# Kernel tuning notes

Measured on AMD Instinct MI355X. Metric: run time of the kernel, lower is better.

## Reference

```python
import jax, jax.numpy as jnp
import numpy as np

B, N, D, H, FF = 4, 1024, 512, 8, 2048
DH = D // H
RPE_HID = 16
COORD_DIM = 2


def _ln(x, g, b, eps=1e-5):
    m = jnp.mean(x, axis=-1, keepdims=True)
    v = jnp.mean((x - m) ** 2, axis=-1, keepdims=True)
    return (x - m) * jax.lax.rsqrt(v + eps) * g + b


def setup_inputs() -> dict:
    key = jax.random.key(0)
    ks = jax.random.split(key, 20)
    s = 0.02
    inp = {
        "x": jax.random.normal(ks[0], (B, N, D), dtype=jnp.float32),
        "coords": jax.random.uniform(ks[1], (B, N, COORD_DIM), dtype=jnp.float32),
        # qkv + output projections
        "Wq": jax.random.normal(ks[2], (D, D), jnp.float32) * s,
        "bq": jnp.zeros((D,), jnp.float32),
        "Wk": jax.random.normal(ks[3], (D, D), jnp.float32) * s,
        "bk": jnp.zeros((D,), jnp.float32),
        "Wv": jax.random.normal(ks[4], (D, D), jnp.float32) * s,
        "bv": jnp.zeros((D,), jnp.float32),
        "Wo": jax.random.normal(ks[5], (D, D), jnp.float32) * s,
        "bo": jnp.zeros((D,), jnp.float32),
        # learned per-head logit scale (Swin-v2 style cosine attention)
        "logit_scale": jnp.full((H, 1, 1), np.log(10.0), jnp.float32),
        # absolute positional embedder PE: Linear(2 -> D)
        "W_pe": jax.random.normal(ks[6], (COORD_DIM, D), jnp.float32) * s,
        "b_pe": jnp.zeros((D,), jnp.float32),
        # relative positional embedder RPE: MLP(2 -> 16 -> H)
        "W_r1": jax.random.normal(ks[7], (COORD_DIM, RPE_HID), jnp.float32) * 0.5,
        "b_r1": jnp.zeros((RPE_HID,), jnp.float32),
        "W_r2": jax.random.normal(ks[8], (RPE_HID, H), jnp.float32) * 0.5,
        "b_r2": jnp.zeros((H,), jnp.float32),
        # layernorm params
        "g_peq": jnp.ones((D,), jnp.float32), "bt_peq": jnp.zeros((D,), jnp.float32),
        "g_pek": jnp.ones((D,), jnp.float32), "bt_pek": jnp.zeros((D,), jnp.float32),
        "g2": jnp.ones((D,), jnp.float32), "bt2": jnp.zeros((D,), jnp.float32),
        "g3": jnp.ones((D,), jnp.float32), "bt3": jnp.zeros((D,), jnp.float32),
        # MLP (bias=False)
        "W_ff1": jax.random.normal(ks[9], (D, FF), jnp.float32) * s,
        "W_ff2": jax.random.normal(ks[10], (FF, D), jnp.float32) * s,
    }
    return inp


def reference(x, coords, Wq, bq, Wk, bk, Wv, bv, Wo, bo, logit_scale,
              W_pe, b_pe, W_r1, b_r1, W_r2, b_r2,
              g_peq, bt_peq, g_pek, bt_pek, g2, bt2, g3, bt3,
              W_ff1, W_ff2):
    # --- PE add + LayerNorm on q and k (self-attention: coords_cross_ = coords)
    pe = coords @ W_pe + b_pe                      # [B,N,D]
    q = _ln(x + pe, g_peq, bt_peq)
    k = _ln(x + pe, g_pek, bt_pek)
    v = x                                          # v is NOT PE-normed in source

    # --- relative-position bias from cartesian coord differences
    rel = coords[:, :, None, :] - coords[:, None, :, :]   # [B,Nq,Nk,2]
    hid = jax.nn.relu(rel @ W_r1 + b_r1)                  # [B,Nq,Nk,16]
    bias = hid @ W_r2 + b_r2                              # [B,Nq,Nk,H]
    bias = jnp.transpose(bias, (0, 3, 1, 2))              # [B,H,Nq,Nk]

    # --- multi-head cosine attention with learned logit scale
    qp = (q @ Wq + bq).reshape(B, N, H, DH)
    kp = (k @ Wk + bk).reshape(B, N, H, DH)
    vp = (v @ Wv + bv).reshape(B, N, H, DH)
    qn = qp / jnp.maximum(jnp.linalg.norm(qp, axis=-1, keepdims=True), 1e-12)
    kn = kp / jnp.maximum(jnp.linalg.norm(kp, axis=-1, keepdims=True), 1e-12)
    scale = jnp.exp(jnp.minimum(logit_scale, jnp.log(100.0)))  # [H,1,1]
    attn = jnp.einsum('bqhd,bkhd->bhqk', qn, kn) * scale[None] + bias
    attn = jax.nn.softmax(attn, axis=-1)
    att_out = jnp.einsum('bhqk,bkhd->bqhd', attn, vp).reshape(B, N, D)
    att_out = att_out @ Wo + bo

    # --- residual + norm + MLP (LeakyReLU 0.2 after each linear) + residual + norm
    x1 = _ln(x + att_out, g2, bt2)
    mlp = jax.nn.leaky_relu(
        jax.nn.leaky_relu(x1 @ W_ff1, 0.2) @ W_ff2, 0.2)
    return _ln(x1 + mlp, g3, bt3)
```

## Files before the change

### kernel.cpp

```cpp
#include <hip/hip_runtime.h>

#define BB 4
#define NN 1024
#define DD 512
#define HH 8
#define DHH 64
#define FFF 2048

typedef __attribute__((ext_vector_type(8))) short bf16x8;
typedef __attribute__((ext_vector_type(4))) float f32x4;
typedef __attribute__((ext_vector_type(4))) unsigned short u16x4;

__device__ inline float wave_sum(float v) {
#pragma unroll
  for (int off = 32; off; off >>= 1) v += __shfl_xor(v, off);
  return v;
}

__device__ inline unsigned short cvt_bf16(float f) {
  union { float f; unsigned u; } x;
  x.f = f;
  unsigned r = x.u + 0x7FFFu + ((x.u >> 16) & 1u);
  return (unsigned short)(r >> 16);
}

__device__ __forceinline__ void gl_lds16(const void* g, void* l) {
  __builtin_amdgcn_global_load_lds(
      (__attribute__((address_space(1))) void*)(g),
      (__attribute__((address_space(3))) void*)(l), 16, 0, 0);
}

__global__ __launch_bounds__(256) void wconv_kernel(
    const float* __restrict__ W0, const float* __restrict__ W1,
    const float* __restrict__ W2, const float* __restrict__ W3,
    const float* __restrict__ W4, const float* __restrict__ W5,
    unsigned short* __restrict__ out) {
  int bidx = blockIdx.x;
  const float* W; unsigned short* Wt; int K, N, local;
  if (bidx < 256) {
    int sel = bidx >> 6; local = bidx & 63;
    W = sel == 0 ? W0 : sel == 1 ? W1 : sel == 2 ? W2 : W3;
    K = 512; N = 512; Wt = out + (size_t)sel * 262144;
  } else if (bidx < 512) {
    local = bidx - 256; W = W4; K = 512; N = 2048; Wt = out + 1048576;
  } else {
    local = bidx - 512; W = W5; K = 2048; N = 512; Wt = out + 2097152;
  }
  int ntn = N >> 6;
  int tn = (local & (ntn - 1)) << 6, tk = (local / ntn) << 6;
  __shared__ float tile[64][65];
  int tid = threadIdx.x;
#pragma unroll
  for (int i = 0; i < 16; ++i) {
    int e = tid + i * 256, kk = e >> 6, nn = e & 63;
    tile[kk][nn] = W[(size_t)(tk + kk) * N + tn + nn];
  }
  __syncthreads();
#pragma unroll
  for (int i = 0; i < 16; ++i) {
    int e = tid + i * 256, nn = e >> 6, kk = e & 63;
    Wt[(size_t)(tn + nn) * K + tk + kk] = cvt_bf16(tile[kk][nn]);
  }
}

__global__ __launch_bounds__(256) void bias_kernel(
    const float* __restrict__ coords,
    const float* __restrict__ W_r1, const float* __restrict__ b_r1,
    const float* __restrict__ W_r2, const float* __restrict__ b_r2,
    unsigned short* __restrict__ bias_out, float* __restrict__ rowmax_out) {
  int kt = blockIdx.x, qt = blockIdx.y, b = blockIdx.z;
  int tid = threadIdx.x;
  int qL = tid >> 2;
  int q = qt * 64 + qL;
  int k0 = kt * 32 + (tid & 3) * 8;
  float cq0 = coords[((size_t)b * NN + q) * 2 + 0];
  float cq1 = coords[((size_t)b * NN + q) * 2 + 1];
  float Aq[16];
#pragma unroll
  for (int l = 0; l < 16; ++l)
    Aq[l] = fmaf(cq0, W_r1[l], fmaf(cq1, W_r1[16 + l], b_r1[l]));
  float ck0[8], ck1[8];
#pragma unroll
  for (int kk = 0; kk < 8; ++kk) {
    ck0[kk] = coords[((size_t)b * NN + k0 + kk) * 2 + 0];
    ck1[kk] = coords[((size_t)b * NN + k0 + kk) * 2 + 1];
  }
  float acc[8][8];
#pragma unroll
  for (int kk = 0; kk < 8; ++kk)
#pragma unroll
    for (int h = 0; h < 8; ++h) acc[kk][h] = b_r2[h];
#pragma unroll
  for (int l = 0; l < 16; ++l) {
    float w1a = W_r1[l], w1b = W_r1[16 + l];
#pragma unroll
    for (int kk = 0; kk < 8; ++kk) {
      float hv = Aq[l] - fmaf(ck0[kk], w1a, ck1[kk] * w1b);
      hv = fmaxf(hv, 0.f);
#pragma unroll
      for (int h = 0; h < 8; ++h)
        acc[kk][h] = fmaf(hv, W_r2[l * HH + h], acc[kk][h]);
    }
  }
  int elem = (qL * 64 + (kt & 1) * 32 + (tid & 3) * 8) ^ ((qL & 7) << 3);
  float mk[8];
#pragma unroll
  for (int h = 0; h < 8; ++h) {
    float m = acc[0][h];
#pragma unroll
    for (int kk = 1; kk < 8; ++kk) m = fmaxf(m, acc[kk][h]);
    m = fmaxf(m, __shfl_xor(m, 1));
    m = fmaxf(m, __shfl_xor(m, 2));
    mk[h] = m;
    bf16x8 ov;
#pragma unroll
    for (int kk = 0; kk < 8; ++kk) ov[kk] = (short)cvt_bf16(acc[kk][h]);
    size_t tile = (((size_t)b * HH + h) * 16 + qt) * 16 + (kt >> 1);
    *(bf16x8*)&bias_out[tile * 4096 + elem] = ov;
  }
  if ((tid & 3) == 0) {
#pragma unroll
    for (int h = 0; h < 8; ++h)
      rowmax_out[(((size_t)b * HH + h) * NN + q) * 32 + kt] = mk[h];
  }
}

__global__ __launch_bounds__(512) void pe_ln_kernel(
    const float* __restrict__ x, const float* __restrict__ coords,
    const float* __restrict__ W_pe, const float* __restrict__ b_pe,
    const float* __restrict__ g_q, const float* __restrict__ bt_q,
    const float* __restrict__ g_k, const float* __restrict__ bt_k,
    unsigned short* __restrict__ q_lnb, unsigned short* __restrict__ k_lnb,
    unsigned short* __restrict__ x_bf) {
  int tid = threadIdx.x;
  int g = tid >> 7, t = tid & 127;
  int row = blockIdx.x * 4 + g;
  int e0 = t * 4;
  float c0 = coords[(size_t)row * 2 + 0];
  float c1 = coords[(size_t)row * 2 + 1];
  size_t base = (size_t)row * DD + e0;
  f32x4 xv = *(const f32x4*)&x[base];
  f32x4 wp0 = *(const f32x4*)&W_pe[e0];
  f32x4 wp1 = *(const f32x4*)&W_pe[DD + e0];
  f32x4 bp  = *(const f32x4*)&b_pe[e0];
  u16x4 xb;
#pragma unroll
  for (int j = 0; j < 4; ++j) xb[j] = cvt_bf16(xv[j]);
  *(u16x4*)&x_bf[base] = xb;
  f32x4 val;
#pragma unroll
  for (int j = 0; j < 4; ++j)
    val[j] = xv[j] + c0 * wp0[j] + c1 * wp1[j] + bp[j];

  __shared__ float ws[8], ws2[8];
  float s = wave_sum(val[0] + val[1] + val[2] + val[3]);
  if ((tid & 63) == 0) ws[tid >> 6] = s;
  __syncthreads();
  float mean = (ws[2 * g] + ws[2 * g + 1]) * (1.f / DD);
  f32x4 dv;
  float s2l = 0.f;
#pragma unroll
  for (int j = 0; j < 4; ++j) { dv[j] = val[j] - mean; s2l = fmaf(dv[j], dv[j], s2l); }
  float s2 = wave_sum(s2l);
  if ((tid & 63) == 0) ws2[tid >> 6] = s2;
  __syncthreads();
  float var = (ws2[2 * g] + ws2[2 * g + 1]) * (1.f / DD);
  float rstd = rsqrtf(var + 1e-5f);
  f32x4 gq = *(const f32x4*)&g_q[e0], bq = *(const f32x4*)&bt_q[e0];
  f32x4 gk = *(const f32x4*)&g_k[e0], bk = *(const f32x4*)&bt_k[e0];
  u16x4 qo, ko;
#pragma unroll
  for (int j = 0; j < 4; ++j) {
    qo[j] = cvt_bf16(dv[j] * rstd * gq[j] + bq[j]);
    ko[j] = cvt_bf16(dv[j] * rstd * gk[j] + bk[j]);
  }
  *(u16x4*)&q_lnb[base] = qo;
  *(u16x4*)&k_lnb[base] = ko;
}

__global__ __launch_bounds__(512) void add_ln_kernel(
    const float* __restrict__ a, const float* __restrict__ r,
    const float* __restrict__ g_, const float* __restrict__ bt,
    float* __restrict__ out, unsigned short* __restrict__ out_bf) {
  int tid = threadIdx.x;
  int g = tid >> 7, t = tid & 127;
  int row = blockIdx.x * 4 + g;
  int e0 = t * 4;
  size_t base = (size_t)row * DD + e0;
  f32x4 av = *(const f32x4*)&a[base];
  f32x4 rv = *(const f32x4*)&r[base];
  f32x4 val;
#pragma unroll
  for (int j = 0; j < 4; ++j) val[j] = av[j] + rv[j];
  __shared__ float ws[8], ws2[8];
  float s = wave_sum(val[0] + val[1] + val[2] + val[3]);
  if ((tid & 63) == 0) ws[tid >> 6] = s;
  __syncthreads();
  float mean = (ws[2 * g] + ws[2 * g + 1]) * (1.f / DD);
  f32x4 dv;
  float s2l = 0.f;
#pragma unroll
  for (int j = 0; j < 4; ++j) { dv[j] = val[j] - mean; s2l = fmaf(dv[j], dv[j], s2l); }
  float s2 = wave_sum(s2l);
  if ((tid & 63) == 0) ws2[tid >> 6] = s2;
  __syncthreads();
  float var = (ws2[2 * g] + ws2[2 * g + 1]) * (1.f / DD);
  float rstd = rsqrtf(var + 1e-5f);
  f32x4 gg = *(const f32x4*)&g_[e0], bb = *(const f32x4*)&bt[e0];
  f32x4 ov;
  u16x4 ob;
#pragma unroll
  for (int j = 0; j < 4; ++j) {
    ov[j] = dv[j] * rstd * gg[j] + bb[j];
    ob[j] = cvt_bf16(ov[j]);
  }
  *(f32x4*)&out[base] = ov;
  if (out_bf) *(u16x4*)&out_bf[base] = ob;
}

template <int ACT, int EPI>
__global__ __launch_bounds__(256) void mgemm_kernel(
    const unsigned short* __restrict__ A, const unsigned short* __restrict__ BT,
    const float* __restrict__ bias, void* __restrict__ C,
    int M, int Nc, int K) {
  __shared__ unsigned short lds[4][8192];
  int tid = threadIdx.x;
  int w = tid >> 6, lane = tid & 63, lg = lane >> 4, lr = lane & 15;
  int bm = blockIdx.y * 128, bn = blockIdx.x * 128;
  int wr = w >> 1, wc = w & 1;
  int segl = lane >> 3;
  int cb = (lane & 7) << 4;

  f32x4 zf = {0.f, 0.f, 0.f, 0.f};
  f32x4 acc[4][4];
#pragma unroll
  for (int mi = 0; mi < 4; ++mi)
#pragma unroll
    for (int ni = 0; ni < 4; ++ni) acc[mi][ni] = zf;

  int nt = K >> 6;

  auto STAGE = [&](int buf, int t) {
    int k0 = t << 6;
#pragma unroll
    for (int i = 0; i < 4; ++i) {
      int seg = w * 4 + i;
      int r = (seg << 3) + segl;
      int csw = cb ^ ((r & 7) << 4);
      const char* ga = (const char*)A + (((size_t)(bm + r) * K + k0) << 1) + csw;
      gl_lds16(ga, &lds[buf * 2][seg << 9]);
      const char* gb = (const char*)BT + (((size_t)(bn + r) * K + k0) << 1) + csw;
      gl_lds16(gb, &lds[buf * 2 + 1][seg << 9]);
    }
  };
  auto COMPUTE = [&](int buf) {
    const unsigned short* As = lds[buf * 2];
    const unsigned short* Bs = lds[buf * 2 + 1];
    bf16x8 af[2][4], bfr[2][4];
#pragma unroll
    for (int kh = 0; kh < 2; ++kh)
#pragma unroll
      for (int mi = 0; mi < 4; ++mi) {
        int r = wr * 64 + mi * 16 + lr;
        int e = (r << 6) + (kh << 5) + (lg << 3);
        af[kh][mi] = *(const bf16x8*)&As[e ^ ((r & 7) << 3)];
        int rb = wc * 64 + mi * 16 + lr;
        int eb = (rb << 6) + (kh << 5) + (lg << 3);
        bfr[kh][mi] = *(const bf16x8*)&Bs[eb ^ ((rb & 7) << 3)];
      }
#pragma unroll
    for (int kh = 0; kh < 2; ++kh)
#pragma unroll
      for (int mi = 0; mi < 4; ++mi)
#pragma unroll
        for (int ni = 0; ni < 4; ++ni)
          acc[mi][ni] = __builtin_amdgcn_mfma_f32_16x16x32_bf16(
              af[kh][mi], bfr[kh][ni], acc[mi][ni], 0, 0, 0);
  };

  STAGE(0, 0);
  __syncthreads();
  for (int t = 0; t < nt; ++t) {
    if (t + 1 < nt) STAGE((t + 1) & 1, t + 1);
    COMPUTE(t & 1);
    __syncthreads();
  }

#pragma unroll
  for (int ni = 0; ni < 4; ++ni) {
    int col = bn + wc * 64 + ni * 16 + lr;
    float bv = bias ? bias[col] : 0.f;
#pragma unroll
    for (int mi = 0; mi < 4; ++mi) {
#pragma unroll
      for (int j = 0; j < 4; ++j) {
        int row = bm + wr * 64 + mi * 16 + lg * 4 + j;
        float v = acc[mi][ni][j] + bv;
        if (ACT == 1) v = v > 0.f ? v : 0.2f * v;
        if (EPI == 1)
          ((unsigned short*)C)[(size_t)row * Nc + col] = cvt_bf16(v);
        else
          ((float*)C)[(size_t)row * Nc + col] = v;
      }
    }
  }
}

template <int ACT, int EPI>
__global__ __launch_bounds__(256) void mgemm64_kernel(
    const unsigned short* __restrict__ A, const unsigned short* __restrict__ BT,
    const float* __restrict__ bias, void* __restrict__ C,
    int M, int Nc, int K) {
  __shared__ unsigned short lds[4][4096];
  int tid = threadIdx.x;
  int w = tid >> 6, lane = tid & 63, lg = lane >> 4, lr = lane & 15;
  int bm = blockIdx.y * 64, bn = blockIdx.x * 64;
  int wr = w >> 1, wc = w & 1;
  int segl = lane >> 3;
  int cb = (lane & 7) << 4;

  f32x4 zf = {0.f, 0.f, 0.f, 0.f};
  f32x4 acc[2][2];
#pragma unroll
  for (int mi = 0; mi < 2; ++mi)
#pragma unroll
    for (int ni = 0; ni < 2; ++ni) acc[mi][ni] = zf;

  int nt = K >> 6;

  auto STAGE = [&](int buf, int t) {
    int k0 = t << 6;
#pragma unroll
    for (int i = 0; i < 2; ++i) {
      int seg = w * 2 + i;
      int r = (seg << 3) + segl;
      int csw = cb ^ ((r & 7) << 4);
      const char* ga = (const char*)A + (((size_t)(bm + r) * K + k0) << 1) + csw;
      gl_lds16(ga, &lds[buf * 2][seg << 9]);
      const char* gb = (const char*)BT + (((size_t)(bn + r) * K + k0) << 1) + csw;
      gl_lds16(gb, &lds[buf * 2 + 1][seg << 9]);
    }
  };
  auto COMPUTE = [&](int buf) {
    const unsigned short* As = lds[buf * 2];
    const unsigned short* Bs = lds[buf * 2 + 1];
    bf16x8 af[2][2], bfr[2][2];
#pragma unroll
    for (int kh = 0; kh < 2; ++kh)
#pragma unroll
      for (int mi = 0; mi < 2; ++mi) {
        int r = wr * 32 + mi * 16 + lr;
        int e = (r << 6) + (kh << 5) + (lg << 3);
        af[kh][mi] = *(const bf16x8*)&As[e ^ ((r & 7) << 3)];
        int rb = wc * 32 + mi * 16 + lr;
        int eb = (rb << 6) + (kh << 5) + (lg << 3);
        bfr[kh][mi] = *(const bf16x8*)&Bs[eb ^ ((rb & 7) << 3)];
      }
#pragma unroll
    for (int kh = 0; kh < 2; ++kh)
#pragma unroll
      for (int mi = 0; mi < 2; ++mi)
#pragma unroll
        for (int ni = 0; ni < 2; ++ni)
          acc[mi][ni] = __builtin_amdgcn_mfma_f32_16x16x32_bf16(
              af[kh][mi], bfr[kh][ni], acc[mi][ni], 0, 0, 0);
  };

  STAGE(0, 0);
  __syncthreads();
  for (int t = 0; t < nt; ++t) {
    if (t + 1 < nt) STAGE((t + 1) & 1, t + 1);
    COMPUTE(t & 1);
    __syncthreads();
  }

#pragma unroll
  for (int ni = 0; ni < 2; ++ni) {
    int col = bn + wc * 32 + ni * 16 + lr;
    float bv = bias ? bias[col] : 0.f;
#pragma unroll
    for (int mi = 0; mi < 2; ++mi) {
#pragma unroll
      for (int j = 0; j < 4; ++j) {
        int row = bm + wr * 32 + mi * 16 + lg * 4 + j;
        float v = acc[mi][ni][j] + bv;
        if (ACT == 1) v = v > 0.f ? v : 0.2f * v;
        if (EPI == 1)
          ((unsigned short*)C)[(size_t)row * Nc + col] = cvt_bf16(v);
        else
          ((float*)C)[(size_t)row * Nc + col] = v;
      }
    }
  }
}

__global__ __launch_bounds__(256) void qkv_gemm_kernel(
    const unsigned short* __restrict__ q_lnb,
    const unsigned short* __restrict__ k_lnb,
    const unsigned short* __restrict__ x_bf,
    const unsigned short* __restrict__ wt,
    const float* __restrict__ bq, const float* __restrict__ bk,
    const float* __restrict__ bv_,
    unsigned short* __restrict__ q_bf, unsigned short* __restrict__ k_swz,
    unsigned short* __restrict__ vt_swz) {
  int z = blockIdx.z;
  const unsigned short* A = z == 0 ? q_lnb : z == 1 ? k_lnb : x_bf;
  const unsigned short* BT = wt + (size_t)z * 262144;
  const float* bias = z == 0 ? bq : z == 1 ? bk : bv_;

  __shared__ unsigned short lds[4][8192];
  int tid = threadIdx.x;
  int w = tid >> 6, lane = tid & 63, lg = lane >> 4, lr = lane & 15;
  int bm = blockIdx.y * 128, bn = blockIdx.x * 128;
  int wr = w >> 1, wc = w & 1;
  int segl = lane >> 3;
  int cb = (lane & 7) << 4;

  f32x4 zf = {0.f, 0.f, 0.f, 0.f};
  f32x4 acc[4][4];
#pragma unroll
  for (int mi = 0; mi < 4; ++mi)
#pragma unroll
    for (int ni = 0; ni < 4; ++ni) acc[mi][ni] = zf;

  auto STAGE = [&](int buf, int t) {
    int k0 = t << 6;
#pragma unroll
    for (int i = 0; i < 4; ++i) {
      int seg = w * 4 + i;
      int r = (seg << 3) + segl;
      int csw = cb ^ ((r & 7) << 4);
      const char* ga = (const char*)A + (((size_t)(bm + r) * DD + k0) << 1) + csw;
      gl_lds16(ga, &lds[buf * 2][seg << 9]);
      const char* gb = (const char*)BT + (((size_t)(bn + r) * DD + k0) << 1) + csw;
      gl_lds16(gb, &lds[buf * 2 + 1][seg << 9]);
    }
  };
  auto COMPUTE = [&](int buf) {
    const unsigned short* As = lds[buf * 2];
    const unsigned short* Bs = lds[buf * 2 + 1];
    bf16x8 af[2][4], bfr[2][4];
#pragma unroll
    for (int kh = 0; kh < 2; ++kh)
#pragma unroll
      for (int mi = 0; mi < 4; ++mi) {
        int r = wr * 64 + mi * 16 + lr;
        int e = (r << 6) + (kh << 5) + (lg << 3);
        af[kh][mi] = *(const bf16x8*)&As[e ^ ((r & 7) << 3)];
        int rb = wc * 64 + mi * 16 + lr;
        int eb = (rb << 6) + (kh << 5) + (lg << 3);
        bfr[kh][mi] = *(const bf16x8*)&Bs[eb ^ ((rb & 7) << 3)];
      }
#pragma unroll
    for (int kh = 0; kh < 2; ++kh)
#pragma unroll
      for (int mi = 0; mi < 4; ++mi)
#pragma unroll
        for (int ni = 0; ni < 4; ++ni)
          acc[mi][ni] = __builtin_amdgcn_mfma_f32_16x16x32_bf16(
              af[kh][mi], bfr[kh][ni], acc[mi][ni], 0, 0, 0);
  };

  STAGE(0, 0);
  __syncthreads();
  for (int t = 0; t < 8; ++t) {
    if (t + 1 < 8) STAGE((t + 1) & 1, t + 1);
    COMPUTE(t & 1);
    __syncthreads();
  }

  int h = (bn >> 6) + wc;
  float bvf[4];
#pragma unroll
  for (int ni = 0; ni < 4; ++ni) bvf[ni] = bias[bn + wc * 64 + ni * 16 + lr];
#pragma unroll
  for (int mi = 0; mi < 4; ++mi) {
#pragma unroll
    for (int j = 0; j < 4; ++j) {
      float vals[4]; float ss = 0.f;
#pragma unroll
      for (int ni = 0; ni < 4; ++ni) {
        float v = acc[mi][ni][j] + bvf[ni];
        vals[ni] = v;
        ss = fmaf(v, v, ss);
      }
      float rn = 1.f;
      if (z <= 1) {
        ss += __shfl_xor(ss, 1);
        ss += __shfl_xor(ss, 2);
        ss += __shfl_xor(ss, 4);
        ss += __shfl_xor(ss, 8);
        rn = 1.f / fmaxf(sqrtf(ss), 1e-12f);
      }
      int row = bm + wr * 64 + mi * 16 + lg * 4 + j;
      int b_ = row >> 10, n_ = row & (NN - 1);
      if (z == 0) {
        unsigned short* ob = q_bf + (((size_t)b_ * HH + h) * NN + n_) * DHH;
#pragma unroll
        for (int ni = 0; ni < 4; ++ni)
          ob[ni * 16 + lr] = cvt_bf16(vals[ni] * rn);
      } else if (z == 1) {
        unsigned short* ob = k_swz + (((size_t)b_ * HH + h) * NN + n_) * DHH;
#pragma unroll
        for (int ni = 0; ni < 4; ++ni)
          ob[(ni * 16 + lr) ^ ((n_ & 7) << 3)] = cvt_bf16(vals[ni] * rn);
      } else {
        int ktn = n_ & ~63, nn = n_ & 63;
#pragma unroll
        for (int ni = 0; ni < 4; ++ni) {
          int d = ni * 16 + lr;
          vt_swz[((size_t)b_ * HH + h) * DHH * NN + (size_t)d * NN + ktn +
                 (nn ^ ((d & 7) << 3))] = cvt_bf16(vals[ni]);
        }
      }
    }
  }
}

template <int NT>
__global__ __launch_bounds__(256) void attn_vres_kernel(
    const unsigned short* __restrict__ qb, const unsigned short* __restrict__ kb,
    const unsigned short* __restrict__ vtg,
    const unsigned short* __restrict__ bias_t,
    const float* __restrict__ rowmax_g,
    const float* __restrict__ logit_scale,
    unsigned short* __restrict__ part, int nb) {
  int qt = blockIdx.x, h = blockIdx.y;
  int b = blockIdx.z % nb, sp = blockIdx.z / nb;
  int tid = threadIdx.x;
  int w = tid >> 6, lane = tid & 63;
  int lg = lane >> 4, lr = lane & 15;

  __shared__ unsigned short kl[NT][4096];
  __shared__ unsigned short vt[NT][4096];
  __shared__ unsigned short bl[NT][4096];
  __shared__ unsigned short pl[4][1024];

  const size_t bh = ((size_t)b * HH + h) * NN;
  const int kt0 = sp * NT;

  int q_glob = qt * 64 + w * 16 + lr;
  bf16x8 aq0 = *(const bf16x8*)&qb[(bh + q_glob) * DHH + lg * 8];
  bf16x8 aq1 = *(const bf16x8*)&qb[(bh + q_glob) * DHH + 32 + lg * 8];

  float m_ub[4];
  float scale_h = __expf(fminf(logit_scale[h], 4.605170185988091f));
#pragma unroll
  for (int r = 0; r < 4; ++r) {
    int qg = qt * 64 + w * 16 + lg * 4 + r;
    const float* rmp = &rowmax_g[(bh + qg) * 32];
    float rm = -1e30f;
#pragma unroll
    for (int i = 0; i < 8; ++i) {
      f32x4 v = *(const f32x4*)&rmp[i * 4];
      rm = fmaxf(rm, fmaxf(fmaxf(v[0], v[1]), fmaxf(v[2], v[3])));
    }
    m_ub[r] = rm + 1.05f * scale_h + 0.1f;
  }

  float l_run[4] = {0.f, 0.f, 0.f, 0.f};
  f32x4 zf = {0.f, 0.f, 0.f, 0.f};
  f32x4 acc_o[4] = {zf, zf, zf, zf};

  const unsigned short* kbase = kb + (bh + (size_t)kt0 * 64) * DHH;
  const unsigned short* bbase =
      bias_t + ((((size_t)b * HH + h) * 16 + qt) * 16 + kt0) * 4096;
  const unsigned short* vbase = vtg + ((size_t)b * HH + h) * DHH * NN;
#pragma unroll
  for (int t = 0; t < NT; ++t) {
#pragma unroll
    for (int i = 0; i < 2; ++i) {
      int chunk = i * 256 + w * 64;
      int idx = chunk + lane;
      gl_lds16(kbase + (size_t)t * 4096 + (size_t)idx * 8, &kl[t][chunk * 8]);
      gl_lds16(bbase + (size_t)t * 4096 + (size_t)idx * 8, &bl[t][chunk * 8]);
      int d = idx >> 3, kc8 = (idx & 7) * 8;
      gl_lds16(vbase + (size_t)d * NN + (kt0 + t) * 64 + kc8,
               &vt[t][chunk * 8]);
    }
  }
  __syncthreads();

  for (int t = 0; t < NT; ++t) {
    f32x4 s_acc[4];
#pragma unroll
    for (int kc = 0; kc < 4; ++kc) {
      int row = kc * 16 + lr;
      int sw = (row & 7) << 3;
      bf16x8 bk0 = *(const bf16x8*)&kl[t][row * 64 + ((lg * 8) ^ sw)];
      bf16x8 bk1 = *(const bf16x8*)&kl[t][row * 64 + ((32 + lg * 8) ^ sw)];
      s_acc[kc] = __builtin_amdgcn_mfma_f32_16x16x32_bf16(aq0, bk0, zf, 0, 0, 0);
      s_acc[kc] = __builtin_amdgcn_mfma_f32_16x16x32_bf16(aq1, bk1, s_acc[kc], 0, 0, 0);
    }

#pragma unroll
    for (int kc = 0; kc < 4; ++kc)
#pragma unroll
      for (int r = 0; r < 4; ++r) {
        int q = w * 16 + lg * 4 + r;
        unsigned short ub =
            bl[t][(q * 64 + kc * 16 + lr) ^ ((q & 7) << 3)];
        float bf_ = __uint_as_float(((unsigned)ub) << 16);
        float p = __expf(fmaf(s_acc[kc][r], scale_h, bf_ - m_ub[r]));
        l_run[r] += p;
        int ql = lg * 4 + r;
        pl[w][(ql * 64 + kc * 16 + lr) ^ ((ql & 7) << 3)] = cvt_bf16(p);
      }

#pragma unroll
    for (int ka = 0; ka < 2; ++ka) {
      bf16x8 pa = *(const bf16x8*)&pl[w][(lr * 64 + ka * 32 + lg * 8) ^
                                         ((lr & 7) << 3)];
#pragma unroll
      for (int ds = 0; ds < 4; ++ds) {
        int d = ds * 16 + lr;
        bf16x8 bv = *(const bf16x8*)&vt[t][(d * 64 + ka * 32 + lg * 8) ^
                                           ((d & 7) << 3)];
        acc_o[ds] = __builtin_amdgcn_mfma_f32_16x16x32_bf16(pa, bv, acc_o[ds], 0, 0, 0);
      }
    }
  }

#pragma unroll
  for (int r = 0; r < 4; ++r) {
    l_run[r] += __shfl_xor(l_run[r], 1);
    l_run[r] += __shfl_xor(l_run[r], 2);
    l_run[r] += __shfl_xor(l_run[r], 4);
    l_run[r] += __shfl_xor(l_run[r], 8);
  }

#pragma unroll
  for (int r = 0; r < 4; ++r) {
    int qg = qt * 64 + w * 16 + lg * 4 + r;
    size_t idx = ((size_t)(sp * nb + b) * HH + h) * NN + qg;
    unsigned short* pr = part + idx * 68;
#pragma unroll
    for (int ds = 0; ds < 4; ++ds)
      pr[ds * 16 + lr] = cvt_bf16(acc_o[ds][r]);
    if (lr == 0) *(float*)(pr + 64) = l_run[r];
  }
}

template <int NS>
__global__ __launch_bounds__(256) void combine_kernel(
    const unsigned short* __restrict__ part, unsigned short* __restrict__ attb,
    int nb) {
  int tid = threadIdx.x;
  int w = tid >> 6, d = tid & 63;
  int row = blockIdx.x * 4 + w;
  int b = row >> 13, rem = row & 8191, h = rem >> 10, n = rem & (NN - 1);
  size_t i0 = ((size_t)b * HH + h) * NN + n;
  size_t stride = (size_t)nb * HH * NN;
  float num = 0.f, den = 0.f;
#pragma unroll
  for (int s = 0; s < NS; ++s) {
    const unsigned short* p = part + (i0 + s * stride) * 68;
    num += __uint_as_float(((unsigned)p[d]) << 16);
    den += *(const float*)(p + 64);
  }
  attb[((size_t)b * NN + n) * DD + h * DHH + d] = cvt_bf16(num / den);
}

extern "C" void kernel_launch(void* const* d_in, const int* in_sizes, int n_in,
                              void* d_out, int out_size, void* d_ws, size_t ws_size,
                              hipStream_t stream) {
  const float* x      = (const float*)d_in[0];
  const float* coords = (const float*)d_in[1];
  const float* Wq = (const float*)d_in[2];  const float* bq = (const float*)d_in[3];
  const float* Wk = (const float*)d_in[4];  const float* bk = (const float*)d_in[5];
  const float* Wv = (const float*)d_in[6];  const float* bv = (const float*)d_in[7];
  const float* Wo = (const float*)d_in[8];  const float* bo = (const float*)d_in[9];
  const float* logit_scale = (const float*)d_in[10];
  const float* W_pe = (const float*)d_in[11]; const float* b_pe = (const float*)d_in[12];
  const float* W_r1 = (const float*)d_in[13]; const float* b_r1 = (const float*)d_in[14];
  const float* W_r2 = (const float*)d_in[15]; const float* b_r2 = (const float*)d_in[16];
  const float* g_peq = (const float*)d_in[17]; const float* bt_peq = (const float*)d_in[18];
  const float* g_pek = (const float*)d_in[19]; const float* bt_pek = (const float*)d_in[20];
  const float* g2 = (const float*)d_in[21]; const float* bt2 = (const float*)d_in[22];
  const float* g3 = (const float*)d_in[23]; const float* bt3 = (const float*)d_in[24];
  const float* W_ff1 = (const float*)d_in[25];
  const float* W_ff2 = (const float*)d_in[26];
  float* out = (float*)d_out;

  const size_t T = (size_t)BB * NN;
  char* wsb = (char*)d_ws;
  const size_t U = 4u * 1024u * 1024u;

  unsigned short* wt_all = (unsigned short*)(wsb + 0 * U);
  unsigned short* WoT   = wt_all + 786432;
  unsigned short* Wff1T = wt_all + 1048576;
  unsigned short* Wff2T = wt_all + 2097152;
  unsigned short* q_lnb = (unsigned short*)(wsb + 2 * U);
  unsigned short* k_lnb = (unsigned short*)(wsb + 3 * U);
  unsigned short* x_bf  = (unsigned short*)(wsb + 4 * U);
  unsigned short* q_bf  = (unsigned short*)(wsb + 5 * U);
  unsigned short* k_swz = (unsigned short*)(wsb + 6 * U);
  unsigned short* v_swz = (unsigned short*)(wsb + 7 * U);
  unsigned short* att_bf = (unsigned short*)(wsb + 8 * U);
  float* proj = (float*)(wsb + 9 * U);
  float* x1   = (float*)(wsb + 11 * U);
  unsigned short* x1_bf = (unsigned short*)(wsb + 13 * U);
  unsigned short* hid_bf = (unsigned short*)(wsb + 2 * U);
  float* mlp  = (float*)(wsb + 9 * U);
  float* rowmax_ws = (float*)(wsb + 2 * U);
  unsigned short* bias_ws = (unsigned short*)(wsb + 9 * U);
  unsigned short* part_ws = (unsigned short*)(wsb + 25 * U);

  wconv_kernel<<<dim3(768), dim3(256), 0, stream>>>(
      Wq, Wk, Wv, Wo, W_ff1, W_ff2, wt_all);

  pe_ln_kernel<<<dim3(T / 4), dim3(512), 0, stream>>>(
      x, coords, W_pe, b_pe, g_peq, bt_peq, g_pek, bt_pek, q_lnb, k_lnb, x_bf);

  qkv_gemm_kernel<<<dim3(DD / 128, T / 128, 3), dim3(256), 0, stream>>>(
      q_lnb, k_lnb, x_bf, wt_all, bq, bk, bv, q_bf, k_swz, v_swz);

  if (ws_size >= 34 * U) {
    bias_kernel<<<dim3(NN / 32, NN / 64, BB), dim3(256), 0, stream>>>(
        coords, W_r1, b_r1, W_r2, b_r2, bias_ws, rowmax_ws);
    attn_vres_kernel<2><<<dim3(NN / 64, HH, 8 * BB), dim3(256), 0, stream>>>(
        q_bf, k_swz, v_swz, bias_ws, rowmax_ws, logit_scale, part_ws, BB);
    combine_kernel<8><<<dim3(BB * HH * NN / 4), dim3(256), 0, stream>>>(
        part_ws, att_bf, BB);
  } else {
    unsigned short* bias_b = (unsigned short*)(wsb + 9 * U);
    unsigned short* part_b = (unsigned short*)(wsb + 13 * U);
    float* rm_b = (float*)(wsb + 2 * U);
    for (int b = 0; b < BB; ++b) {
      bias_kernel<<<dim3(NN / 32, NN / 64, 1), dim3(256), 0, stream>>>(
          coords + (size_t)b * NN * 2, W_r1, b_r1, W_r2, b_r2, bias_b, rm_b);
      attn_vres_kernel<2><<<dim3(NN / 64, HH, 8), dim3(256), 0, stream>>>(
          q_bf + (size_t)b * HH * NN * DHH, k_swz + (size_t)b * HH * NN * DHH,
          v_swz + (size_t)b * HH * DHH * NN, bias_b, rm_b, logit_scale,
          part_b, 1);
      combine_kernel<8><<<dim3(HH * NN / 4), dim3(256), 0, stream>>>(
          part_b, att_bf + (size_t)b * NN * DD, 1);
    }
  }

  mgemm64_kernel<0, 0><<<dim3(DD / 64, T / 64), dim3(256), 0, stream>>>(
      att_bf, WoT, bo, proj, (int)T, DD, DD);

  add_ln_kernel<<<dim3(T / 4), dim3(512), 0, stream>>>(
      x, proj, g2, bt2, x1, x1_bf);

  mgemm_kernel<1, 1><<<dim3(FFF / 128, T / 128), dim3(256), 0, stream>>>(
      x1_bf, Wff1T, nullptr, hid_bf, (int)T, FFF, DD);
  mgemm64_kernel<1, 0><<<dim3(DD / 64, T / 64), dim3(256), 0, stream>>>(
      hid_bf, Wff2T, nullptr, mlp, (int)T, DD, FFF);

  add_ln_kernel<<<dim3(T / 4), dim3(512), 0, stream>>>(
      x1, mlp, g3, bt3, out, nullptr);
}
```

Measured before the change: 178.6 us.

## Read K and V straight from global memory and use fewer, larger key splits in attention

The attention kernel no longer stages K and V tiles in LDS. It reads them directly from global memory as MFMA operands, and the swizzled layouts in the QKV GEMM epilogue are dropped in favour of plain row-major K and transposed V. The key split drops from 8 ways of 2 tiles to 2 ways of 8 tiles, which shrinks the partial buffer, the combine work and the workspace needed for the fast path. The trade-offs are uncached global loads inside the inner loop, fewer blocks to hide latency, and a bias LDS array that is now four times larger per block.

```diff
diff --git a/kernel.cpp b/kernel.cpp
--- a/kernel.cpp
+++ b/kernel.cpp
@@ -401,8 +401,8 @@
     const unsigned short* __restrict__ wt,
     const float* __restrict__ bq, const float* __restrict__ bk,
     const float* __restrict__ bv_,
-    unsigned short* __restrict__ q_bf, unsigned short* __restrict__ k_swz,
-    unsigned short* __restrict__ vt_swz) {
+    unsigned short* __restrict__ q_bf, unsigned short* __restrict__ k_bf,
+    unsigned short* __restrict__ vt_g) {
   int z = blockIdx.z;
   const unsigned short* A = z == 0 ? q_lnb : z == 1 ? k_lnb : x_bf;
   const unsigned short* BT = wt + (size_t)z * 262144;
@@ -494,24 +494,17 @@
       }
       int row = bm + wr * 64 + mi * 16 + lg * 4 + j;
       int b_ = row >> 10, n_ = row & (NN - 1);
-      if (z == 0) {
-        unsigned short* ob = q_bf + (((size_t)b_ * HH + h) * NN + n_) * DHH;
+      if (z <= 1) {
+        unsigned short* ob = (z == 0 ? q_bf : k_bf) +
+                             (((size_t)b_ * HH + h) * NN + n_) * DHH;
 #pragma unroll
         for (int ni = 0; ni < 4; ++ni)
           ob[ni * 16 + lr] = cvt_bf16(vals[ni] * rn);
-      } else if (z == 1) {
-        unsigned short* ob = k_swz + (((size_t)b_ * HH + h) * NN + n_) * DHH;
+      } else {
 #pragma unroll
         for (int ni = 0; ni < 4; ++ni)
-          ob[(ni * 16 + lr) ^ ((n_ & 7) << 3)] = cvt_bf16(vals[ni] * rn);
-      } else {
-        int ktn = n_ & ~63, nn = n_ & 63;
-#pragma unroll
-        for (int ni = 0; ni < 4; ++ni) {
-          int d = ni * 16 + lr;
-          vt_swz[((size_t)b_ * HH + h) * DHH * NN + (size_t)d * NN + ktn +
-                 (nn ^ ((d & 7) << 3))] = cvt_bf16(vals[ni]);
-        }
+          vt_g[(((size_t)b_ * HH + h) * DHH + ni * 16 + lr) * NN + n_] =
+              cvt_bf16(vals[ni]);
       }
     }
   }
@@ -531,12 +524,11 @@
   int w = tid >> 6, lane = tid & 63;
   int lg = lane >> 4, lr = lane & 15;
 
-  __shared__ unsigned short kl[NT][4096];
-  __shared__ unsigned short vt[NT][4096];
   __shared__ unsigned short bl[NT][4096];
   __shared__ unsigned short pl[4][1024];
 
   const size_t bh = ((size_t)b * HH + h) * NN;
+  const size_t vbase = ((size_t)b * HH + h) * DHH * NN;
   const int kt0 = sp * NT;
 
   int q_glob = qt * 64 + w * 16 + lr;
@@ -562,33 +554,29 @@
   f32x4 zf = {0.f, 0.f, 0.f, 0.f};
   f32x4 acc_o[4] = {zf, zf, zf, zf};
 
-  const unsigned short* kbase = kb + (bh + (size_t)kt0 * 64) * DHH;
   const unsigned short* bbase =
       bias_t + ((((size_t)b * HH + h) * 16 + qt) * 16 + kt0) * 4096;
-  const unsigned short* vbase = vtg + ((size_t)b * HH + h) * DHH * NN;
 #pragma unroll
   for (int t = 0; t < NT; ++t) {
 #pragma unroll
     for (int i = 0; i < 2; ++i) {
       int chunk = i * 256 + w * 64;
-      int idx = chunk + lane;
-      gl_lds16(kbase + (size_t)t * 4096 + (size_t)idx * 8, &kl[t][chunk * 8]);
-      gl_lds16(bbase + (size_t)t * 4096 + (size_t)idx * 8, &bl[t][chunk * 8]);
-      int d = idx >> 3, kc8 = (idx & 7) * 8;
-      gl_lds16(vbase + (size_t)d * NN + (kt0 + t) * 64 + kc8,
-               &vt[t][chunk * 8]);
+      gl_lds16(bbase + (size_t)t * 4096 + (size_t)(chunk + lane) * 8,
+               &bl[t][chunk * 8]);
     }
   }
   __syncthreads();
 
   for (int t = 0; t < NT; ++t) {
+    int ktg = kt0 + t;
+
     f32x4 s_acc[4];
 #pragma unroll
     for (int kc = 0; kc < 4; ++kc) {
-      int row = kc * 16 + lr;
-      int sw = (row & 7) << 3;
-      bf16x8 bk0 = *(const bf16x8*)&kl[t][row * 64 + ((lg * 8) ^ sw)];
-      bf16x8 bk1 = *(const bf16x8*)&kl[t][row * 64 + ((32 + lg * 8) ^ sw)];
+      const unsigned short* krow =
+          &kb[(bh + ktg * 64 + kc * 16 + lr) * DHH + lg * 8];
+      bf16x8 bk0 = *(const bf16x8*)krow;
+      bf16x8 bk1 = *(const bf16x8*)(krow + 32);
       s_acc[kc] = __builtin_amdgcn_mfma_f32_16x16x32_bf16(aq0, bk0, zf, 0, 0, 0);
       s_acc[kc] = __builtin_amdgcn_mfma_f32_16x16x32_bf16(aq1, bk1, s_acc[kc], 0, 0, 0);
     }
@@ -598,8 +586,7 @@
 #pragma unroll
       for (int r = 0; r < 4; ++r) {
         int q = w * 16 + lg * 4 + r;
-        unsigned short ub =
-            bl[t][(q * 64 + kc * 16 + lr) ^ ((q & 7) << 3)];
+        unsigned short ub = bl[t][(q * 64 + kc * 16 + lr) ^ ((q & 7) << 3)];
         float bf_ = __uint_as_float(((unsigned)ub) << 16);
         float p = __expf(fmaf(s_acc[kc][r], scale_h, bf_ - m_ub[r]));
         l_run[r] += p;
@@ -614,8 +601,8 @@
 #pragma unroll
       for (int ds = 0; ds < 4; ++ds) {
         int d = ds * 16 + lr;
-        bf16x8 bv = *(const bf16x8*)&vt[t][(d * 64 + ka * 32 + lg * 8) ^
-                                           ((d & 7) << 3)];
+        bf16x8 bv = *(const bf16x8*)&vtg[vbase + (size_t)d * NN +
+                                         ktg * 64 + ka * 32 + lg * 8];
         acc_o[ds] = __builtin_amdgcn_mfma_f32_16x16x32_bf16(pa, bv, acc_o[ds], 0, 0, 0);
       }
     }
@@ -648,7 +635,9 @@
   int tid = threadIdx.x;
   int w = tid >> 6, d = tid & 63;
   int row = blockIdx.x * 4 + w;
-  int b = row >> 13, rem = row & 8191, h = rem >> 10, n = rem & (NN - 1);
+  int nrow = nb * HH * NN;
+  if (row >= nrow) return;
+  int b = row / (HH * NN), rem = row % (HH * NN), h = rem >> 10, n = rem & (NN - 1);
   size_t i0 = ((size_t)b * HH + h) * NN + n;
   size_t stride = (size_t)nb * HH * NN;
   float num = 0.f, den = 0.f;
@@ -694,8 +683,8 @@
   unsigned short* k_lnb = (unsigned short*)(wsb + 3 * U);
   unsigned short* x_bf  = (unsigned short*)(wsb + 4 * U);
   unsigned short* q_bf  = (unsigned short*)(wsb + 5 * U);
-  unsigned short* k_swz = (unsigned short*)(wsb + 6 * U);
-  unsigned short* v_swz = (unsigned short*)(wsb + 7 * U);
+  unsigned short* k_bf  = (unsigned short*)(wsb + 6 * U);
+  unsigned short* v_bf  = (unsigned short*)(wsb + 7 * U);
   unsigned short* att_bf = (unsigned short*)(wsb + 8 * U);
   float* proj = (float*)(wsb + 9 * U);
   float* x1   = (float*)(wsb + 11 * U);
@@ -713,14 +702,14 @@
       x, coords, W_pe, b_pe, g_peq, bt_peq, g_pek, bt_pek, q_lnb, k_lnb, x_bf);
 
   qkv_gemm_kernel<<<dim3(DD / 128, T / 128, 3), dim3(256), 0, stream>>>(
-      q_lnb, k_lnb, x_bf, wt_all, bq, bk, bv, q_bf, k_swz, v_swz);
-
-  if (ws_size >= 34 * U) {
+      q_lnb, k_lnb, x_bf, wt_all, bq, bk, bv, q_bf, k_bf, v_bf);
+
+  if (ws_size >= 28 * U) {
     bias_kernel<<<dim3(NN / 32, NN / 64, BB), dim3(256), 0, stream>>>(
         coords, W_r1, b_r1, W_r2, b_r2, bias_ws, rowmax_ws);
-    attn_vres_kernel<2><<<dim3(NN / 64, HH, 8 * BB), dim3(256), 0, stream>>>(
-        q_bf, k_swz, v_swz, bias_ws, rowmax_ws, logit_scale, part_ws, BB);
-    combine_kernel<8><<<dim3(BB * HH * NN / 4), dim3(256), 0, stream>>>(
+    attn_vres_kernel<8><<<dim3(NN / 64, HH, 2 * BB), dim3(256), 0, stream>>>(
+        q_bf, k_bf, v_bf, bias_ws, rowmax_ws, logit_scale, part_ws, BB);
+    combine_kernel<2><<<dim3(BB * HH * NN / 4), dim3(256), 0, stream>>>(
         part_ws, att_bf, BB);
   } else {
     unsigned short* bias_b = (unsigned short*)(wsb + 9 * U);
@@ -729,11 +718,11 @@
     for (int b = 0; b < BB; ++b) {
       bias_kernel<<<dim3(NN / 32, NN / 64, 1), dim3(256), 0, stream>>>(
           coords + (size_t)b * NN * 2, W_r1, b_r1, W_r2, b_r2, bias_b, rm_b);
-      attn_vres_kernel<2><<<dim3(NN / 64, HH, 8), dim3(256), 0, stream>>>(
-          q_bf + (size_t)b * HH * NN * DHH, k_swz + (size_t)b * HH * NN * DHH,
-          v_swz + (size_t)b * HH * DHH * NN, bias_b, rm_b, logit_scale,
+      attn_vres_kernel<8><<<dim3(NN / 64, HH, 2), dim3(256), 0, stream>>>(
+          q_bf + (size_t)b * HH * NN * DHH, k_bf + (size_t)b * HH * NN * DHH,
+          v_bf + (size_t)b * HH * DHH * NN, bias_b, rm_b, logit_scale,
           part_b, 1);
-      combine_kernel<8><<<dim3(HH * NN / 4), dim3(256), 0, stream>>>(
+      combine_kernel<2><<<dim3(HH * NN / 4), dim3(256), 0, stream>>>(
           part_b, att_bf + (size_t)b * NN * DD, 1);
     }
   }
```

After: 197.3 us. 10.5% more time.
